# Optimization experiments

Measured on AMD Instinct MI355X. Metric: run time of the kernel, lower is better.

The kernel has to match this reference:

```python
import jax, jax.numpy as jnp
import numpy as np

B, N, M, D = 32, 500, 500, 256
SQRT_D = 16.0
LOGIT_CLIP = 10.0


def setup_inputs() -> dict:
    key = jax.random.key(0)
    ks = jax.random.split(key, 12)
    s = 1.0 / np.sqrt(D)
    return {
        "encoded_q0": jax.random.normal(ks[0], (B, N, D), jnp.float32),
        "encoded_jobs": jax.random.normal(ks[1], (B, M, D), jnp.float32),
        "encoded_q1": jax.random.normal(ks[2], (B, N, D), jnp.float32),
        "cur_cost_mat": jax.random.uniform(ks[3], (B, N, M), jnp.float32),
        "log_scale": jnp.ones((1,), jnp.float32),
        "ninf_mask": jnp.zeros((B, N, M), jnp.float32),
        "Wq0": jax.random.normal(ks[4], (D, D), jnp.float32) * s,
        "Wq1": jax.random.normal(ks[5], (D, D), jnp.float32) * s,
        "Wk": jax.random.normal(ks[6], (D, D), jnp.float32) * s,
        "Wv": jax.random.normal(ks[7], (D, D), jnp.float32) * s,
        "alpha1": jnp.ones((1,), jnp.float32),
        "alpha2": jnp.ones((1,), jnp.float32),
    }


def reference(encoded_q0, encoded_jobs, encoded_q1, cur_cost_mat, log_scale,
              ninf_mask, Wq0, Wq1, Wk, Wv, alpha1, alpha2):
    # precomputed state (set_kv / set_q1): Linear without bias -> x @ W.T
    k = jnp.einsum('bmd,ed->bme', encoded_jobs, Wk)
    v = jnp.einsum('bmd,ed->bme', encoded_jobs, Wv)
    q1 = jnp.einsum('bnd,ed->bne', encoded_q1, Wq1)
    q0 = jnp.einsum('bnd,ed->bne', encoded_q0, Wq0)
    q = q1 + q0

    # AAFM: adaptation bias = -alpha1 * log_scale * cost (+ ninf_mask)
    exp_bias = jnp.exp(-alpha1 * log_scale * cur_cost_mat + ninf_mask)  # (B,N,M)
    exp_k = jnp.exp(k)                                                   # (B,M,D)
    num = jnp.einsum('bnm,bmd->bnd', exp_bias, exp_k * v)
    den = jnp.einsum('bnm,bmd->bnd', exp_bias, exp_k)
    weighted = jnp.nan_to_num(num / den)
    aafm_out = jax.nn.sigmoid(q) * weighted                              # (B,N,D)

    # single-head scoring against raw encoded_jobs
    score = jnp.einsum('bnd,bmd->bnm', aafm_out, encoded_jobs)
    score = score / SQRT_D - alpha2 * log_scale * cur_cost_mat
    score = LOGIT_CLIP * jnp.tanh(score) + ninf_mask
    return jax.nn.softmax(score, axis=-1)
```

## Files before the change

### kernel.cpp

```cpp
#include <hip/hip_runtime.h>
#include <math.h>

using u16 = unsigned short;
typedef __attribute__((ext_vector_type(8))) short short8;
typedef __attribute__((ext_vector_type(16))) float floatx16;

constexpr int Bc = 32, Nn = 500, Mm = 500, Dd = 256;
constexpr float LOGIT_CLIP = 10.0f;
constexpr float INV_SQRT_D = 1.0f / 16.0f;

__device__ __forceinline__ floatx16 mfma32(short8 a, short8 b, floatx16 c) {
    return __builtin_amdgcn_mfma_f32_32x32x16_bf16(a, b, c, 0, 0, 0);
}

__device__ __forceinline__ floatx16 zero16() {
    floatx16 v = {0.f,0.f,0.f,0.f,0.f,0.f,0.f,0.f,0.f,0.f,0.f,0.f,0.f,0.f,0.f,0.f};
    return v;
}

__device__ __forceinline__ void split1(float x, u16& h, u16& l) {
    unsigned u = __float_as_uint(x);
    unsigned rh = (u + 0x7FFFu + ((u >> 16) & 1u)) & 0xFFFF0000u;
    float fh = __uint_as_float(rh);
    float fl = x - fh;
    unsigned ul = __float_as_uint(fl);
    unsigned rl = ul + 0x7FFFu + ((ul >> 16) & 1u);
    h = (u16)(rh >> 16);
    l = (u16)(rl >> 16);
}

__device__ __forceinline__ u16 bf16rtn(float x) {
    unsigned u = __float_as_uint(x);
    return (u16)((u + 0x7FFFu + ((u >> 16) & 1u)) >> 16);
}

__device__ __forceinline__ float fast_tanh(float x) {
    return 1.0f - 2.0f / (__expf(2.0f * x) + 1.0f);
}

__device__ __forceinline__ void split8(const float4& a, const float4& c,
                                       short8& hv, short8& lv) {
    u16 hh, ll;
    split1(a.x, hh, ll); hv[0] = (short)hh; lv[0] = (short)ll;
    split1(a.y, hh, ll); hv[1] = (short)hh; lv[1] = (short)ll;
    split1(a.z, hh, ll); hv[2] = (short)hh; lv[2] = (short)ll;
    split1(a.w, hh, ll); hv[3] = (short)hh; lv[3] = (short)ll;
    split1(c.x, hh, ll); hv[4] = (short)hh; lv[4] = (short)ll;
    split1(c.y, hh, ll); hv[5] = (short)hh; lv[5] = (short)ll;
    split1(c.z, hh, ll); hv[6] = (short)hh; lv[6] = (short)ll;
    split1(c.w, hh, ll); hv[7] = (short)hh; lv[7] = (short)ll;
}


__global__ __launch_bounds__(256) void k0w_pk(const float* __restrict__ s0,
                                              const float* __restrict__ s1,
                                              const float* __restrict__ s2,
                                              const float* __restrict__ s3,
                                              u16* __restrict__ pkw) {
    const float* s = blockIdx.y == 0 ? s0 : blockIdx.y == 1 ? s1 :
                     blockIdx.y == 2 ? s2 : s3;
    const int w = blockIdx.y;
    const int flat = (blockIdx.x * 256 + threadIdx.x) * 8;
    const int i = flat >> 8, j0 = flat & 255;
    float4 a = *(const float4*)&s[flat];
    float4 c = *(const float4*)&s[flat + 4];
    short8 hv, lv;
    split8(a, c, hv, lv);
    const int dt = i >> 5, i31 = i & 31, dc = j0 >> 4, hp = (j0 >> 3) & 1;
    const size_t off = (size_t)(w * 8 + dt) * 16384 + (size_t)dc * 1024
                     + (size_t)((hp << 5) | i31) * 8;
    *(short8*)&pkw[off] = hv;
    *(short8*)&pkw[off + 512] = lv;
}

__global__ __launch_bounds__(256) void k0pk3(const float* __restrict__ s0,
                                             const float* __restrict__ s1,
                                             const float* __restrict__ s2,
                                             u16* __restrict__ d0,
                                             u16* __restrict__ d1,
                                             u16* __restrict__ d2) {
    const float* s = blockIdx.y == 0 ? s0 : blockIdx.y == 1 ? s1 : s2;
    u16* d = blockIdx.y == 0 ? d0 : blockIdx.y == 1 ? d1 : d2;
    const int bx = blockIdx.x;
    const int b = bx >> 6;
    const int chunk = bx & 63;
    const int flat = threadIdx.x * 8;
    const int lr = flat >> 8;
    const int j0 = flat & 255;
    const int pr = chunk * 8 + lr;
    short8 hv = {0,0,0,0,0,0,0,0}, lv = {0,0,0,0,0,0,0,0};
    if (pr < Nn) {
        const size_t o = ((size_t)b * Nn + pr) * Dd + j0;
        float4 a = *(const float4*)&s[o];
        float4 c = *(const float4*)&s[o + 4];
        split8(a, c, hv, lv);
    }
    const int mt = pr >> 5, r31 = pr & 31;
    const int dc = j0 >> 4, hp = (j0 >> 3) & 1;
    const size_t off = (size_t)(b * 16 + mt) * 16384 + (size_t)dc * 1024
                     + (size_t)((hp << 5) | r31) * 8;
    *(short8*)&d[off] = hv;
    *(short8*)&d[off + 512] = lv;
}

__global__ __launch_bounds__(256) void kexp_pk(const float* __restrict__ cost,
                                               const float* __restrict__ mask,
                                               const float* __restrict__ alpha1,
                                               const float* __restrict__ lsc,
                                               u16* __restrict__ pka) {
    __shared__ u16 tile[32][520];
    const float a1ls = alpha1[0] * lsc[0];
    const int b = blockIdx.x >> 4, nt = blockIdx.x & 15;
    const int t = threadIdx.x;
#pragma unroll
    for (int q = 0; q < 8; ++q) {
        const int flat = (q << 11) + (t << 3);
        const int nl = flat >> 9, m = flat & 511;
        const int n = min(nt * 32 + nl, Nn - 1);
        const size_t o = ((size_t)b * Nn + n) * Mm + m;
        ushort4 w0 = {0, 0, 0, 0}, w1 = {0, 0, 0, 0};
        if (m <= 488) {
            float4 c0 = *(const float4*)&cost[o];
            float4 c1 = *(const float4*)&cost[o + 4];
            float4 k0 = *(const float4*)&mask[o];
            float4 k1 = *(const float4*)&mask[o + 4];
            w0.x = bf16rtn(__expf(fmaf(-a1ls, c0.x, k0.x)));
            w0.y = bf16rtn(__expf(fmaf(-a1ls, c0.y, k0.y)));
            w0.z = bf16rtn(__expf(fmaf(-a1ls, c0.z, k0.z)));
            w0.w = bf16rtn(__expf(fmaf(-a1ls, c0.w, k0.w)));
            w1.x = bf16rtn(__expf(fmaf(-a1ls, c1.x, k1.x)));
            w1.y = bf16rtn(__expf(fmaf(-a1ls, c1.y, k1.y)));
            w1.z = bf16rtn(__expf(fmaf(-a1ls, c1.z, k1.z)));
            w1.w = bf16rtn(__expf(fmaf(-a1ls, c1.w, k1.w)));
        } else if (m == 496) {
            float4 c0 = *(const float4*)&cost[o];
            float4 k0 = *(const float4*)&mask[o];
            w0.x = bf16rtn(__expf(fmaf(-a1ls, c0.x, k0.x)));
            w0.y = bf16rtn(__expf(fmaf(-a1ls, c0.y, k0.y)));
            w0.z = bf16rtn(__expf(fmaf(-a1ls, c0.z, k0.z)));
            w0.w = bf16rtn(__expf(fmaf(-a1ls, c0.w, k0.w)));
        }
        *(ushort4*)&tile[nl][m] = w0;
        *(ushort4*)&tile[nl][m + 4] = w1;
    }
    __syncthreads();
    const int lane = t & 63, wvv = t >> 6;
    const int n31 = lane & 31, hh = lane >> 5;
    const size_t pbase = (size_t)(b * 16 + nt) * 16384 + (size_t)lane * 8;
#pragma unroll
    for (int q = 0; q < 8; ++q) {
        const int mc = wvv * 8 + q;
        short8 v = *(const short8*)&tile[n31][mc * 16 + hh * 8];
        *(short8*)&pka[pbase + (size_t)mc * 512] = v;
    }
}

__global__ __launch_bounds__(256) void k1_kv(const u16* __restrict__ pkj,
                                             const u16* __restrict__ pkw,
                                             u16* __restrict__ pkb) {
    const int lane = threadIdx.x & 63, wv = threadIdx.x >> 6;
    const int l31 = lane & 31, h = lane >> 5;
    const int b = blockIdx.z;
    const int dt = blockIdx.y * 4 + wv;
    const int mt = blockIdx.x;
    const int M0 = mt * 32;

    const size_t wk  = (size_t)dt * 16384 + (size_t)lane * 8;
    const size_t wvb = (size_t)(8 + dt) * 16384 + (size_t)lane * 8;
    const size_t jb  = (size_t)(b * 16 + mt) * 16384 + (size_t)lane * 8;

    floatx16 ak = zero16(), av = zero16();

    short8 buf[3][6];
#define K1L(S, DC) { \
    buf[S][0] = *(const short8*)(pkw + wk  + (size_t)(DC) * 1024); \
    buf[S][1] = *(const short8*)(pkw + wk  + (size_t)(DC) * 1024 + 512); \
    buf[S][2] = *(const short8*)(pkw + wvb + (size_t)(DC) * 1024); \
    buf[S][3] = *(const short8*)(pkw + wvb + (size_t)(DC) * 1024 + 512); \
    buf[S][4] = *(const short8*)(pkj + jb  + (size_t)(DC) * 1024); \
    buf[S][5] = *(const short8*)(pkj + jb  + (size_t)(DC) * 1024 + 512); }

    K1L(0, 0)
    K1L(1, 1)
#pragma unroll
    for (int it = 0; it < 16; ++it) {
        if (it + 2 < 16) { K1L((it + 2) % 3, it + 2) }
        const int c = it % 3;
        ak = mfma32(buf[c][0], buf[c][4], ak);
        ak = mfma32(buf[c][0], buf[c][5], ak);
        ak = mfma32(buf[c][1], buf[c][4], ak);
        av = mfma32(buf[c][2], buf[c][4], av);
        av = mfma32(buf[c][2], buf[c][5], av);
        av = mfma32(buf[c][3], buf[c][4], av);
    }
#undef K1L

    const int hp = (l31 >> 3) & 1, ee = l31 & 7, mcl = l31 >> 4;
    const size_t sb0 = ((size_t)b * 8 + dt) * 65536
                     + (size_t)(mt * 2 + mcl) * 2048 + (size_t)hp * 256 + ee;
    const bool v0 = (M0 + l31) < Mm;
#pragma unroll
    for (int r = 0; r < 16; ++r) {
        const int d31 = (r & 3) + ((r >> 2) << 3) + (h << 2);
        const size_t o = sb0 + (size_t)d31 * 8;
        u16 hh, ll;
        const float ek = v0 ? __expf(ak[r]) : 0.f;
        const float ev = v0 ? ek * av[r] : 0.f;
        split1(ek, hh, ll); pkb[o] = hh; pkb[o + 512] = ll;
        split1(ev, hh, ll); pkb[o + 1024] = hh; pkb[o + 1536] = ll;
    }
}

__global__ __launch_bounds__(256) void k2_q(const u16* __restrict__ pkq0,
                                            const u16* __restrict__ pkq1,
                                            const u16* __restrict__ pkw,
                                            float* __restrict__ sq) {
    const int lane = threadIdx.x & 63, wv = threadIdx.x >> 6;
    const int l31 = lane & 31, h = lane >> 5;
    const int b = blockIdx.y;
    const int nt = blockIdx.x;
    const int N0 = nt * 32;
    const int dt0 = wv;
    const int dt1 = wv + 4;

    const size_t qa  = (size_t)(b * 16 + nt) * 16384 + (size_t)lane * 8;
    const size_t w00 = (size_t)(16 + dt0) * 16384 + (size_t)lane * 8;
    const size_t w10 = (size_t)(24 + dt0) * 16384 + (size_t)lane * 8;
    const size_t w01 = (size_t)(16 + dt1) * 16384 + (size_t)lane * 8;
    const size_t w11 = (size_t)(24 + dt1) * 16384 + (size_t)lane * 8;

    floatx16 acc0 = zero16(), acc1 = zero16();

    short8 buf[3][12];
#define K2L(S, DC) { \
    buf[S][0]  = *(const short8*)(pkq0 + qa + (size_t)(DC) * 1024); \
    buf[S][1]  = *(const short8*)(pkq0 + qa + (size_t)(DC) * 1024 + 512); \
    buf[S][2]  = *(const short8*)(pkq1 + qa + (size_t)(DC) * 1024); \
    buf[S][3]  = *(const short8*)(pkq1 + qa + (size_t)(DC) * 1024 + 512); \
    buf[S][4]  = *(const short8*)(pkw + w00 + (size_t)(DC) * 1024); \
    buf[S][5]  = *(const short8*)(pkw + w00 + (size_t)(DC) * 1024 + 512); \
    buf[S][6]  = *(const short8*)(pkw + w10 + (size_t)(DC) * 1024); \
    buf[S][7]  = *(const short8*)(pkw + w10 + (size_t)(DC) * 1024 + 512); \
    buf[S][8]  = *(const short8*)(pkw + w01 + (size_t)(DC) * 1024); \
    buf[S][9]  = *(const short8*)(pkw + w01 + (size_t)(DC) * 1024 + 512); \
    buf[S][10] = *(const short8*)(pkw + w11 + (size_t)(DC) * 1024); \
    buf[S][11] = *(const short8*)(pkw + w11 + (size_t)(DC) * 1024 + 512); }

    K2L(0, 0)
    K2L(1, 1)
#pragma unroll
    for (int it = 0; it < 16; ++it) {
        if (it + 2 < 16) { K2L((it + 2) % 3, it + 2) }
        const int c = it % 3;
        acc0 = mfma32(buf[c][0], buf[c][4], acc0);
        acc0 = mfma32(buf[c][0], buf[c][5], acc0);
        acc0 = mfma32(buf[c][1], buf[c][4], acc0);
        acc0 = mfma32(buf[c][2], buf[c][6], acc0);
        acc0 = mfma32(buf[c][2], buf[c][7], acc0);
        acc0 = mfma32(buf[c][3], buf[c][6], acc0);
        acc1 = mfma32(buf[c][0], buf[c][8], acc1);
        acc1 = mfma32(buf[c][0], buf[c][9], acc1);
        acc1 = mfma32(buf[c][1], buf[c][8], acc1);
        acc1 = mfma32(buf[c][2], buf[c][10], acc1);
        acc1 = mfma32(buf[c][2], buf[c][11], acc1);
        acc1 = mfma32(buf[c][3], buf[c][10], acc1);
    }
#undef K2L

#pragma unroll
    for (int r = 0; r < 16; ++r) {
        const int n = N0 + (r & 3) + ((r >> 2) << 3) + (h << 2);
        if (n < Nn) {
            const size_t o = ((size_t)b * Nn + n) * Dd + l31;
            sq[o + dt0 * 32] = 1.0f / (1.0f + __expf(-acc0[r]));
            sq[o + dt1 * 32] = 1.0f / (1.0f + __expf(-acc1[r]));
        }
    }
}

__global__ __launch_bounds__(256) void k3_aafm(const u16* __restrict__ pka,
                                               const u16* __restrict__ pkb,
                                               const float* __restrict__ sq,
                                               u16* __restrict__ pkc) {
    const int i = blockIdx.x;
    const int x = i & 7, j = i >> 3;
    const int nt = j & 15;
    const int dh = (j >> 4) & 1;
    const int b = ((j >> 5) << 3) + x;
    const int lane = threadIdx.x & 63, wv = threadIdx.x >> 6;
    const int l31 = lane & 31, h = lane >> 5;
    const int N0 = nt << 5;
    const int dt = dh * 4 + wv;

    const size_t abase = (size_t)(b * 16 + nt) * 16384 + (size_t)lane * 8;
    const size_t bb = ((size_t)b * 8 + dt) * 65536 + (size_t)lane * 8;

    floatx16 dn = zero16(), nm = zero16();

    short8 buf[3][5];
#define K3L(S, MC) { \
    buf[S][0] = *(const short8*)(pka + abase + (size_t)(MC) * 512); \
    buf[S][1] = *(const short8*)(pkb + bb + (size_t)(MC) * 2048); \
    buf[S][2] = *(const short8*)(pkb + bb + (size_t)(MC) * 2048 + 512); \
    buf[S][3] = *(const short8*)(pkb + bb + (size_t)(MC) * 2048 + 1024); \
    buf[S][4] = *(const short8*)(pkb + bb + (size_t)(MC) * 2048 + 1536); }

    K3L(0, 0)
    K3L(1, 1)
#pragma unroll
    for (int it = 0; it < 32; ++it) {
        if (it + 2 < 32) { K3L((it + 2) % 3, it + 2) }
        const int c = it % 3;
        dn = mfma32(buf[c][0], buf[c][1], dn);
        dn = mfma32(buf[c][0], buf[c][2], dn);
        nm = mfma32(buf[c][0], buf[c][3], nm);
        nm = mfma32(buf[c][0], buf[c][4], nm);
    }
#undef K3L

    const int hp = (l31 >> 3) & 1, ee = l31 & 7;
    const int dcol = dt * 32 + l31;
    const int dc0 = dcol >> 4;
    const size_t cb0 = (size_t)(b * 16 + nt) * 16384 + (size_t)dc0 * 1024
                     + (size_t)hp * 256 + ee;
#pragma unroll
    for (int r = 0; r < 16; ++r) {
        const int n31 = (r & 3) + ((r >> 2) << 3) + (h << 2);
        const int n = N0 + n31;
        if (n < Nn) {
            const size_t so = ((size_t)b * Nn + n) * Dd + dcol;
            const size_t o = cb0 + (size_t)n31 * 8;
            u16 hh, ll;
            const float d0 = dn[r];
            const float w0 = (d0 != 0.f) ? nm[r] / d0 : 0.f;
            split1(sq[so] * w0, hh, ll);
            pkc[o] = hh; pkc[o + 512] = ll;
        }
    }
}

__global__ __launch_bounds__(512) void k4_score(const u16* __restrict__ pkc,
                                                const u16* __restrict__ pkj,
                                                const float* __restrict__ cost,
                                                const float* __restrict__ mask,
                                                const float* __restrict__ alpha2,
                                                const float* __restrict__ lsc,
                                                float* __restrict__ out) {
    __shared__ float pred[32][8];
    const int i = blockIdx.x;
    const int x = i & 7, j = i >> 3;
    const int nt = j & 15;
    const int b = ((j >> 4) << 3) + x;
    const int lane = threadIdx.x & 63, wv = threadIdx.x >> 6;
    const int l31 = lane & 31, h = lane >> 5;
    const int N0 = nt << 5;
    const float a2ls = alpha2[0] * lsc[0];

    const size_t ab  = (size_t)(b * 16 + nt) * 16384 + (size_t)lane * 8;
    const size_t jb0 = (size_t)(b * 16 + wv * 2) * 16384 + (size_t)lane * 8;
    const size_t jb1 = jb0 + 16384;
    const int m0g = wv * 64 + l31;
    const int m1g = m0g + 32;

    floatx16 acc0 = zero16(), acc1 = zero16();

    short8 buf[3][6];
#define K4L(S, DC) { \
    buf[S][0] = *(const short8*)(pkc + ab  + (size_t)(DC) * 1024); \
    buf[S][1] = *(const short8*)(pkc + ab  + (size_t)(DC) * 1024 + 512); \
    buf[S][2] = *(const short8*)(pkj + jb0 + (size_t)(DC) * 1024); \
    buf[S][3] = *(const short8*)(pkj + jb0 + (size_t)(DC) * 1024 + 512); \
    buf[S][4] = *(const short8*)(pkj + jb1 + (size_t)(DC) * 1024); \
    buf[S][5] = *(const short8*)(pkj + jb1 + (size_t)(DC) * 1024 + 512); }

    K4L(0, 0)
    K4L(1, 1)
#pragma unroll
    for (int it = 0; it < 16; ++it) {
        if (it + 2 < 16) { K4L((it + 2) % 3, it + 2) }
        const int c = it % 3;
        acc0 = mfma32(buf[c][0], buf[c][2], acc0);
        acc0 = mfma32(buf[c][0], buf[c][3], acc0);
        acc0 = mfma32(buf[c][1], buf[c][2], acc0);
        acc1 = mfma32(buf[c][0], buf[c][4], acc1);
        acc1 = mfma32(buf[c][0], buf[c][5], acc1);
        acc1 = mfma32(buf[c][1], buf[c][4], acc1);
    }
#undef K4L

    float lg0[16], lg1[16];
    const size_t cb = (size_t)b * Nn * Mm;
#pragma unroll
    for (int r = 0; r < 16; ++r) {
        const int row = (r & 3) + ((r >> 2) << 3) + (h << 2);
        const int n = N0 + row;
        if (n < Nn) {
            const size_t o = cb + (size_t)n * Mm + m0g;
            lg0[r] = LOGIT_CLIP * fast_tanh(fmaf(-a2ls, cost[o], acc0[r] * INV_SQRT_D)) + mask[o];
            if (m1g < Mm) {
                const size_t o1 = o + 32;
                lg1[r] = LOGIT_CLIP * fast_tanh(fmaf(-a2ls, cost[o1], acc1[r] * INV_SQRT_D)) + mask[o1];
            } else lg1[r] = -1e30f;
        } else { lg0[r] = -1e30f; lg1[r] = -1e30f; }
    }

    float rm[16];
#pragma unroll
    for (int r = 0; r < 16; ++r) rm[r] = fmaxf(lg0[r], lg1[r]);
#pragma unroll
    for (int d = 1; d < 32; d <<= 1)
#pragma unroll
        for (int r = 0; r < 16; ++r) rm[r] = fmaxf(rm[r], __shfl_xor(rm[r], d));
    if (l31 == 0) {
#pragma unroll
        for (int r = 0; r < 16; ++r)
            pred[(r & 3) + ((r >> 2) << 3) + (h << 2)][wv] = rm[r];
    }
    __syncthreads();
    float fm[16];
#pragma unroll
    for (int r = 0; r < 16; ++r) {
        const int row = (r & 3) + ((r >> 2) << 3) + (h << 2);
        float v = pred[row][0];
#pragma unroll
        for (int w = 1; w < 8; ++w) v = fmaxf(v, pred[row][w]);
        fm[r] = v;
    }
    __syncthreads();

    float sm[16];
#pragma unroll
    for (int r = 0; r < 16; ++r) {
        lg0[r] = __expf(lg0[r] - fm[r]);
        lg1[r] = __expf(lg1[r] - fm[r]);
        sm[r] = lg0[r] + lg1[r];
    }
#pragma unroll
    for (int d = 1; d < 32; d <<= 1)
#pragma unroll
        for (int r = 0; r < 16; ++r) sm[r] += __shfl_xor(sm[r], d);
    if (l31 == 0) {
#pragma unroll
        for (int r = 0; r < 16; ++r)
            pred[(r & 3) + ((r >> 2) << 3) + (h << 2)][wv] = sm[r];
    }
    __syncthreads();

#pragma unroll
    for (int r = 0; r < 16; ++r) {
        const int row = (r & 3) + ((r >> 2) << 3) + (h << 2);
        const int n = N0 + row;
        if (n < Nn) {
            float s = pred[row][0];
#pragma unroll
            for (int w = 1; w < 8; ++w) s += pred[row][w];
            const float inv = 1.0f / s;
            const size_t o = cb + (size_t)n * Mm + m0g;
            out[o] = lg0[r] * inv;
            if (m1g < Mm) out[o + 32] = lg1[r] * inv;
        }
    }
}

extern "C" void kernel_launch(void* const* d_in, const int* in_sizes, int n_in,
                              void* d_out, int out_size, void* d_ws, size_t ws_size,
                              hipStream_t stream) {
    const float* q0        = (const float*)d_in[0];
    const float* jobs      = (const float*)d_in[1];
    const float* q1        = (const float*)d_in[2];
    const float* cost      = (const float*)d_in[3];
    const float* log_scale = (const float*)d_in[4];
    const float* mask      = (const float*)d_in[5];
    const float* Wq0       = (const float*)d_in[6];
    const float* Wq1       = (const float*)d_in[7];
    const float* Wk        = (const float*)d_in[8];
    const float* Wv        = (const float*)d_in[9];
    const float* alpha1    = (const float*)d_in[10];
    const float* alpha2    = (const float*)d_in[11];
    float* out = (float*)d_out;

    const size_t PK_SZ  = (size_t)Bc * 16 * 16384;
    const size_t PKW_SZ = (size_t)4 * 8 * 16384;
    const size_t PKB_SZ = (size_t)Bc * 8 * 65536;

    u16* ws   = (u16*)d_ws;
    u16* pkj  = ws;
    u16* pkq0 = ws + PK_SZ;
    u16* pkq1 = ws + 2 * PK_SZ;
    u16* pkw  = ws + 3 * PK_SZ;
    u16* pkb  = pkw + PKW_SZ;
    float* sq = (float*)(pkb + PKB_SZ);

    u16* pka = pkq1;
    u16* pkc = pkq0;
    (void)ws_size;

    dim3 blk(256);
    k0w_pk<<<dim3(32, 4), blk, 0, stream>>>(Wk, Wv, Wq0, Wq1, pkw);
    k0pk3<<<dim3(2048, 3), blk, 0, stream>>>(jobs, q0, q1, pkj, pkq0, pkq1);
    k1_kv<<<dim3(16, 2, 32), blk, 0, stream>>>(pkj, pkw, pkb);
    k2_q<<<dim3(16, 32), blk, 0, stream>>>(pkq0, pkq1, pkw, sq);
    kexp_pk<<<512, blk, 0, stream>>>(cost, mask, alpha1, log_scale, pka);
    k3_aafm<<<1024, blk, 0, stream>>>(pka, pkb, sq, pkc);
    k4_score<<<512, dim3(512), 0, stream>>>(pkc, pkj, cost, mask,
                                            alpha2, log_scale, out);
}
```

Measured before the change: 295.8 us.

## Stage shared B operands through LDS via direct global-to-LDS loads in k3 and k4

In the AAFM and scoring kernels, the B-operand tiles (exp_k/v packed data, encoded_jobs packed data) are now loaded cooperatively by the whole block into double-buffered shared memory using global_load_lds, instead of each wave loading its own slice from global into registers with a triple-buffered prefetch. The A operand is still loaded per wave with a register double buffer. This aims to cut VGPR pressure and use asynchronous direct-to-LDS transfers. In exchange it adds a __syncthreads per iteration and an LDS footprint, and each wave still reads only its own slice, so there is little data reuse.

```diff
diff --git a/kernel.cpp b/kernel.cpp
--- a/kernel.cpp
+++ b/kernel.cpp
@@ -16,6 +16,12 @@
 __device__ __forceinline__ floatx16 zero16() {
     floatx16 v = {0.f,0.f,0.f,0.f,0.f,0.f,0.f,0.f,0.f,0.f,0.f,0.f,0.f,0.f,0.f,0.f};
     return v;
+}
+
+__device__ __forceinline__ void gl_lds16(const u16* g, u16* l) {
+    __builtin_amdgcn_global_load_lds(
+        (const __attribute__((address_space(1))) unsigned int*)g,
+        (__attribute__((address_space(3))) unsigned int*)l, 16, 0, 0);
 }
 
 __device__ __forceinline__ void split1(float x, u16& h, u16& l) {
@@ -282,41 +288,60 @@
                                                const u16* __restrict__ pkb,
                                                const float* __restrict__ sq,
                                                u16* __restrict__ pkc) {
+    __shared__ u16 bbuf[2][8192];
     const int i = blockIdx.x;
     const int x = i & 7, j = i >> 3;
     const int nt = j & 15;
     const int dh = (j >> 4) & 1;
     const int b = ((j >> 5) << 3) + x;
-    const int lane = threadIdx.x & 63, wv = threadIdx.x >> 6;
+    const int t = threadIdx.x;
+    const int lane = t & 63, wv = t >> 6;
     const int l31 = lane & 31, h = lane >> 5;
     const int N0 = nt << 5;
     const int dt = dh * 4 + wv;
 
+    const u16* pbB = pkb + ((size_t)b * 8 + dh * 4) * 65536;
     const size_t abase = (size_t)(b * 16 + nt) * 16384 + (size_t)lane * 8;
-    const size_t bb = ((size_t)b * 8 + dt) * 65536 + (size_t)lane * 8;
 
     floatx16 dn = zero16(), nm = zero16();
 
-    short8 buf[3][5];
-#define K3L(S, MC) { \
-    buf[S][0] = *(const short8*)(pka + abase + (size_t)(MC) * 512); \
-    buf[S][1] = *(const short8*)(pkb + bb + (size_t)(MC) * 2048); \
-    buf[S][2] = *(const short8*)(pkb + bb + (size_t)(MC) * 2048 + 512); \
-    buf[S][3] = *(const short8*)(pkb + bb + (size_t)(MC) * 2048 + 1024); \
-    buf[S][4] = *(const short8*)(pkb + bb + (size_t)(MC) * 2048 + 1536); }
-
-    K3L(0, 0)
-    K3L(1, 1)
-#pragma unroll
-    for (int it = 0; it < 32; ++it) {
-        if (it + 2 < 32) { K3L((it + 2) % 3, it + 2) }
-        const int c = it % 3;
-        dn = mfma32(buf[c][0], buf[c][1], dn);
-        dn = mfma32(buf[c][0], buf[c][2], dn);
-        nm = mfma32(buf[c][0], buf[c][3], nm);
-        nm = mfma32(buf[c][0], buf[c][4], nm);
-    }
-#undef K3L
+#define STG3(BUF, MC) { \
+    { const int f = 0 * 2048 + t * 8; \
+      gl_lds16(pbB + (size_t)(f >> 11) * 65536 + (size_t)(MC) * 2048 + (f & 2047), \
+               &bbuf[BUF][0 * 2048 + wv * 512]); } \
+    { const int f = 1 * 2048 + t * 8; \
+      gl_lds16(pbB + (size_t)(f >> 11) * 65536 + (size_t)(MC) * 2048 + (f & 2047), \
+               &bbuf[BUF][1 * 2048 + wv * 512]); } \
+    { const int f = 2 * 2048 + t * 8; \
+      gl_lds16(pbB + (size_t)(f >> 11) * 65536 + (size_t)(MC) * 2048 + (f & 2047), \
+               &bbuf[BUF][2 * 2048 + wv * 512]); } \
+    { const int f = 3 * 2048 + t * 8; \
+      gl_lds16(pbB + (size_t)(f >> 11) * 65536 + (size_t)(MC) * 2048 + (f & 2047), \
+               &bbuf[BUF][3 * 2048 + wv * 512]); } }
+
+    STG3(0, 0)
+    short8 aa[2];
+    aa[0] = *(const short8*)(pka + abase);
+    __syncthreads();
+#pragma unroll
+    for (int mc = 0; mc < 32; ++mc) {
+        const int cur = mc & 1, nxt = cur ^ 1;
+        if (mc + 1 < 32) {
+            STG3(nxt, mc + 1)
+            aa[nxt] = *(const short8*)(pka + abase + (size_t)(mc + 1) * 512);
+        }
+        const u16* bp = &bbuf[cur][wv * 2048];
+        short8 ekh = *(const short8*)(bp + (size_t)lane * 8);
+        short8 ekl = *(const short8*)(bp + 512 + (size_t)lane * 8);
+        short8 evh = *(const short8*)(bp + 1024 + (size_t)lane * 8);
+        short8 evl = *(const short8*)(bp + 1536 + (size_t)lane * 8);
+        dn = mfma32(aa[cur], ekh, dn);
+        dn = mfma32(aa[cur], ekl, dn);
+        nm = mfma32(aa[cur], evh, nm);
+        nm = mfma32(aa[cur], evl, nm);
+        __syncthreads();
+    }
+#undef STG3
 
     const int hp = (l31 >> 3) & 1, ee = l31 & 7;
     const int dcol = dt * 32 + l31;
@@ -346,47 +371,66 @@
                                                 const float* __restrict__ alpha2,
                                                 const float* __restrict__ lsc,
                                                 float* __restrict__ out) {
-    __shared__ float pred[32][8];
+    __shared__ u16 bb[2][16384];
+    float (*pred)[8] = (float(*)[8])bb;
     const int i = blockIdx.x;
     const int x = i & 7, j = i >> 3;
     const int nt = j & 15;
     const int b = ((j >> 4) << 3) + x;
-    const int lane = threadIdx.x & 63, wv = threadIdx.x >> 6;
+    const int t = threadIdx.x;
+    const int lane = t & 63, wv = t >> 6;
     const int l31 = lane & 31, h = lane >> 5;
     const int N0 = nt << 5;
     const float a2ls = alpha2[0] * lsc[0];
 
-    const size_t ab  = (size_t)(b * 16 + nt) * 16384 + (size_t)lane * 8;
-    const size_t jb0 = (size_t)(b * 16 + wv * 2) * 16384 + (size_t)lane * 8;
-    const size_t jb1 = jb0 + 16384;
+    const u16* jbB = pkj + (size_t)b * 16 * 16384;
+    const size_t ab = (size_t)(b * 16 + nt) * 16384 + (size_t)lane * 8;
     const int m0g = wv * 64 + l31;
     const int m1g = m0g + 32;
 
     floatx16 acc0 = zero16(), acc1 = zero16();
 
-    short8 buf[3][6];
-#define K4L(S, DC) { \
-    buf[S][0] = *(const short8*)(pkc + ab  + (size_t)(DC) * 1024); \
-    buf[S][1] = *(const short8*)(pkc + ab  + (size_t)(DC) * 1024 + 512); \
-    buf[S][2] = *(const short8*)(pkj + jb0 + (size_t)(DC) * 1024); \
-    buf[S][3] = *(const short8*)(pkj + jb0 + (size_t)(DC) * 1024 + 512); \
-    buf[S][4] = *(const short8*)(pkj + jb1 + (size_t)(DC) * 1024); \
-    buf[S][5] = *(const short8*)(pkj + jb1 + (size_t)(DC) * 1024 + 512); }
-
-    K4L(0, 0)
-    K4L(1, 1)
-#pragma unroll
-    for (int it = 0; it < 16; ++it) {
-        if (it + 2 < 16) { K4L((it + 2) % 3, it + 2) }
-        const int c = it % 3;
-        acc0 = mfma32(buf[c][0], buf[c][2], acc0);
-        acc0 = mfma32(buf[c][0], buf[c][3], acc0);
-        acc0 = mfma32(buf[c][1], buf[c][2], acc0);
-        acc1 = mfma32(buf[c][0], buf[c][4], acc1);
-        acc1 = mfma32(buf[c][0], buf[c][5], acc1);
-        acc1 = mfma32(buf[c][1], buf[c][4], acc1);
-    }
-#undef K4L
+#define STG4(BUF, DC) { \
+    { const int f = 0 * 4096 + t * 8; \
+      gl_lds16(jbB + (size_t)(f >> 10) * 16384 + (size_t)(DC) * 1024 + (f & 1023), \
+               &bb[BUF][0 * 4096 + wv * 512]); } \
+    { const int f = 1 * 4096 + t * 8; \
+      gl_lds16(jbB + (size_t)(f >> 10) * 16384 + (size_t)(DC) * 1024 + (f & 1023), \
+               &bb[BUF][1 * 4096 + wv * 512]); } \
+    { const int f = 2 * 4096 + t * 8; \
+      gl_lds16(jbB + (size_t)(f >> 10) * 16384 + (size_t)(DC) * 1024 + (f & 1023), \
+               &bb[BUF][2 * 4096 + wv * 512]); } \
+    { const int f = 3 * 4096 + t * 8; \
+      gl_lds16(jbB + (size_t)(f >> 10) * 16384 + (size_t)(DC) * 1024 + (f & 1023), \
+               &bb[BUF][3 * 4096 + wv * 512]); } }
+
+    STG4(0, 0)
+    short8 aH[2], aL[2];
+    aH[0] = *(const short8*)(pkc + ab);
+    aL[0] = *(const short8*)(pkc + ab + 512);
+    __syncthreads();
+#pragma unroll
+    for (int dc = 0; dc < 16; ++dc) {
+        const int cur = dc & 1, nxt = cur ^ 1;
+        if (dc + 1 < 16) {
+            STG4(nxt, dc + 1)
+            aH[nxt] = *(const short8*)(pkc + ab + (size_t)(dc + 1) * 1024);
+            aL[nxt] = *(const short8*)(pkc + ab + (size_t)(dc + 1) * 1024 + 512);
+        }
+        const u16* bp = &bb[cur][wv * 2048];
+        short8 b0h = *(const short8*)(bp + (size_t)lane * 8);
+        short8 b0l = *(const short8*)(bp + 512 + (size_t)lane * 8);
+        short8 b1h = *(const short8*)(bp + 1024 + (size_t)lane * 8);
+        short8 b1l = *(const short8*)(bp + 1536 + (size_t)lane * 8);
+        acc0 = mfma32(aH[cur], b0h, acc0);
+        acc0 = mfma32(aH[cur], b0l, acc0);
+        acc0 = mfma32(aL[cur], b0h, acc0);
+        acc1 = mfma32(aH[cur], b1h, acc1);
+        acc1 = mfma32(aH[cur], b1l, acc1);
+        acc1 = mfma32(aL[cur], b1h, acc1);
+        __syncthreads();
+    }
+#undef STG4
 
     float lg0[16], lg1[16];
     const size_t cb = (size_t)b * Nn * Mm;
```

After: 302.2 us. 2.1% more time.
